# Kernel optimization log

Measured on AMD Instinct MI355X. Metric: run time of the kernel, lower is better.

Reference implementation:

```python
import jax, jax.numpy as jnp
import numpy as np

H = 12  # num_heads (ViT-B)


def setup_inputs() -> dict:
    key = jax.random.key(0)
    ks = jax.random.split(key, 16)
    B, N, C = 128, 197, 768
    eff, hd = H // 2, C // H
    d = {
        'x':  jax.random.normal(ks[0], (B, N, C), jnp.float32),
        'Wq': jax.random.normal(ks[1], (C, C), jnp.float32) * 0.02,
        'bq': jax.random.normal(ks[2], (C,), jnp.float32) * 0.02,
        'Wk': jax.random.normal(ks[3], (C, C), jnp.float32) * 0.02,
        'bk': jax.random.normal(ks[4], (C,), jnp.float32) * 0.02,
        'Wv': jax.random.normal(ks[5], (C, C), jnp.float32) * 0.02,
        'bv': jax.random.normal(ks[6], (C,), jnp.float32) * 0.02,
        'Wp': jax.random.normal(ks[7], (C, C), jnp.float32) * 0.02,
        'bp': jax.random.normal(ks[8], (C,), jnp.float32) * 0.02,
        'lq1': jax.random.normal(ks[9],  (eff, 1, hd), jnp.float32) * 0.02,
        'lk1': jax.random.normal(ks[10], (eff, 1, hd), jnp.float32) * 0.02,
        'lq2': jax.random.normal(ks[11], (eff, 1, hd), jnp.float32) * 0.02,
        'lk2': jax.random.normal(ks[12], (eff, 1, hd), jnp.float32) * 0.02,
        'num_heads': 12,
        'lambda_init': jnp.float32(0.8),
    }
    return d


def reference(x, Wq, bq, Wk, bk, Wv, bv, Wp, bp, lq1, lk1, lq2, lk2, num_heads, lambda_init):
    B, N, C = x.shape
    hd = C // num_heads
    scale = hd ** -0.5

    def heads(y):  # [B,N,C] -> [B,H,N,hd]
        return y.reshape(B, N, num_heads, hd).transpose(0, 2, 1, 3)

    q = heads(x @ Wq.T + bq)
    k = heads(x @ Wk.T + bk)
    v = heads(x @ Wv.T + bv)
    eff = num_heads // 2
    q1, q2 = q[:, :eff], q[:, eff:]
    k1, k2 = k[:, :eff], k[:, eff:]
    v1, v2 = v[:, :eff], v[:, eff:]

    l1 = jnp.exp(jnp.minimum((lq1 * lk1).sum((-1, -2)), 5.0))  # [eff]
    l2 = jnp.exp(jnp.minimum((lq2 * lk2).sum((-1, -2)), 5.0))
    lv = (l1 - l2 + lambda_init).mean()  # scalar

    def attn(qh, kh, vh):  # [B,eff,N,hd]
        s = jnp.einsum('bhnd,bhmd->bhnm', qh, kh) * scale
        a = jax.nn.softmax(s, axis=-1)
        o = jnp.einsum('bhnm,bhmd->bhnd', a, vh)
        return o.transpose(0, 2, 1, 3).reshape(B, N, C // 2)

    x1 = attn(q1, k1, v1)
    x2 = attn(q2, k2, v2)
    out = jnp.concatenate([x1 - lv * x2, x2], axis=-1)
    return out @ Wp.T + bp
```

## Files before the change

kernel.cpp:

```cpp
#include <hip/hip_runtime.h>
#include <hip/hip_bf16.h>
#include <stdint.h>


typedef __attribute__((ext_vector_type(4))) float f32x4;
typedef __attribute__((ext_vector_type(8))) short s16x8;
typedef __attribute__((ext_vector_type(8))) __bf16 bf16x8;

typedef const __attribute__((address_space(1))) void* gptr_t;
typedef __attribute__((address_space(3))) void* lptr_t;

__device__ __forceinline__ f32x4 mfma16(s16x8 a, s16x8 b, f32x4 c) {
  return __builtin_amdgcn_mfma_f32_16x16x32_bf16(
      __builtin_bit_cast(bf16x8, a), __builtin_bit_cast(bf16x8, b), c, 0, 0, 0);
}

__device__ __forceinline__ short f2bf(float f) {
  unsigned u = __float_as_uint(f);
  u += 0x7fffu + ((u >> 16) & 1u);
  return (short)(u >> 16);
}
__device__ __forceinline__ float bf2f(short s) {
  return __uint_as_float(((unsigned)(unsigned short)s) << 16);
}

__device__ __forceinline__ void gload_lds16(const void* g, void* l) {
  __builtin_amdgcn_global_load_lds((gptr_t)g, (lptr_t)l, 16, 0, 0);
}

__global__ void cvt_f32_to_bf16(const float* __restrict__ src,
                                short* __restrict__ dst, long n8) {
  long i = (long)blockIdx.x * blockDim.x + threadIdx.x;
  const long stride = (long)gridDim.x * blockDim.x;
  for (; i < n8; i += stride) {
    const float4 a = ((const float4*)src)[2 * i];
    const float4 b = ((const float4*)src)[2 * i + 1];
    s16x8 o;
    o[0] = f2bf(a.x); o[1] = f2bf(a.y); o[2] = f2bf(a.z); o[3] = f2bf(a.w);
    o[4] = f2bf(b.x); o[5] = f2bf(b.y); o[6] = f2bf(b.z); o[7] = f2bf(b.w);
    ((s16x8*)dst)[i] = o;
  }
}

__global__ void lv_kernel(const float* __restrict__ lq1, const float* __restrict__ lk1,
                          const float* __restrict__ lq2, const float* __restrict__ lk2,
                          const float* __restrict__ lambda_init, float* __restrict__ out) {
  const int l = threadIdx.x;
  float v = 0.f;
  if (l < 6) {
    float d1 = 0.f, d2 = 0.f;
    for (int j = 0; j < 64; ++j) {
      d1 += lq1[l * 64 + j] * lk1[l * 64 + j];
      d2 += lq2[l * 64 + j] * lk2[l * 64 + j];
    }
    v = expf(fminf(d1, 5.f)) - expf(fminf(d2, 5.f));
  }
  v += __shfl_xor(v, 1, 64);
  v += __shfl_xor(v, 2, 64);
  v += __shfl_xor(v, 4, 64);
  if (l == 0) out[0] = v * (1.f / 6.f) + lambda_init[0];
}

__global__ void cvt_wp_prime(const float* __restrict__ Wp,
                             const float* __restrict__ lvp,
                             short* __restrict__ dst) {
  const int idx = blockIdx.x * blockDim.x + threadIdx.x;
  if (idx >= 73728) return;
  const float lv = *lvp;
  const int ic = idx % 96;
  const float4 a = ((const float4*)Wp)[2 * idx];
  const float4 b = ((const float4*)Wp)[2 * idx + 1];
  float v[8] = {a.x, a.y, a.z, a.w, b.x, b.y, b.z, b.w};
  if (ic >= 48) {
    const float4 a2 = ((const float4*)Wp)[2 * idx - 96];
    const float4 b2 = ((const float4*)Wp)[2 * idx - 95];
    v[0] -= lv * a2.x; v[1] -= lv * a2.y; v[2] -= lv * a2.z; v[3] -= lv * a2.w;
    v[4] -= lv * b2.x; v[5] -= lv * b2.y; v[6] -= lv * b2.z; v[7] -= lv * b2.w;
  }
  s16x8 o;
#pragma unroll
  for (int j = 0; j < 8; ++j) o[j] = f2bf(v[j]);
  ((s16x8*)dst)[idx] = o;
}

template <int OUT_BF16, int NKT>
__global__ __launch_bounds__(256) void gemm_bt(const short* __restrict__ A, int lda,
                                               const short* __restrict__ B,
                                               const float* __restrict__ bias,
                                               void* __restrict__ C,
                                               int M, int N) {
  const int K = NKT * 64;
  const int nbx = N >> 7;
  const int nwg = gridDim.x;
  const int qq = nwg >> 3, rr = nwg & 7;
  const int xcd = blockIdx.x & 7, pos = blockIdx.x >> 3;
  const int wg = (xcd < rr ? xcd * (qq + 1) : rr * (qq + 1) + (xcd - rr) * qq) + pos;
  const int bx = wg % nbx;
  const int by = wg / nbx;
  const long m0 = (long)by << 7;
  const int n0 = bx << 7;
  __shared__ short Asm[128 * 64];
  __shared__ short Bsm[128 * 64];
  const int tid = threadIdx.x;
  const int lane = tid & 63;
  const int w = tid >> 6;
  const int wr = w >> 1, wc = w & 1;
  const int r16 = lane & 15, g = lane >> 4;

  const short* abase[4];
  const short* bbase[4];
#pragma unroll
  for (int i = 0; i < 4; ++i) {
    const int c = i * 256 + tid;
    const int row = c >> 3;
    const int lc = (c & 7) ^ (row & 7);
    abase[i] = A + (m0 + row) * (long)lda + lc * 8;
    bbase[i] = B + (long)(n0 + row) * (long)K + lc * 8;
  }

  f32x4 acc[4][4];
#pragma unroll
  for (int i = 0; i < 4; ++i)
#pragma unroll
    for (int j = 0; j < 4; ++j) acc[i][j] = f32x4{0.f, 0.f, 0.f, 0.f};

#pragma unroll
  for (int kt = 0; kt < NKT; ++kt) {
    __syncthreads();
#pragma unroll
    for (int i = 0; i < 4; ++i) {
      gload_lds16(abase[i] + kt * 64, Asm + i * 2048 + w * 512);
      gload_lds16(bbase[i] + kt * 64, Bsm + i * 2048 + w * 512);
    }
    asm volatile("s_waitcnt vmcnt(0)" ::: "memory");
    __syncthreads();
#pragma unroll
    for (int kk = 0; kk < 2; ++kk) {
      s16x8 av[4], bvv[4];
#pragma unroll
      for (int f = 0; f < 4; ++f) {
        const int ar = wr * 64 + f * 16 + r16;
        av[f] = *(const s16x8*)(Asm + ar * 64 + ((((kk << 2) + g) ^ (ar & 7)) << 3));
        const int br = wc * 64 + f * 16 + r16;
        bvv[f] = *(const s16x8*)(Bsm + br * 64 + ((((kk << 2) + g) ^ (br & 7)) << 3));
      }
#pragma unroll
      for (int fm = 0; fm < 4; ++fm)
#pragma unroll
        for (int fn = 0; fn < 4; ++fn)
          acc[fm][fn] = mfma16(av[fm], bvv[fn], acc[fm][fn]);
    }
  }
#pragma unroll
  for (int fm = 0; fm < 4; ++fm)
#pragma unroll
    for (int fn = 0; fn < 4; ++fn) {
      const int col = n0 + wc * 64 + fn * 16 + r16;
      const float bb = bias[col];
#pragma unroll
      for (int r = 0; r < 4; ++r) {
        const long row = m0 + wr * 64 + fm * 16 + g * 4 + r;
        const float v = acc[fm][fn][r] + bb;
        if (OUT_BF16) ((short*)C)[row * (long)N + col] = f2bf(v);
        else          ((float*)C)[row * (long)N + col] = v;
      }
    }
}

__global__ __launch_bounds__(512, 4) void attn_kernel(short* QKV) {
  const int b = blockIdx.x / 12;
  const int h = blockIdx.x % 12;
  __shared__ short Ksm[208 * 72];
  __shared__ short Vsm[64 * 232];
  __shared__ short Psm[8][2][512];
  const int tid = threadIdx.x;
  const long base = (long)b * 197 * 2304;

  for (int c = tid; c < 208 * 8; c += 512) {
    const int key = c >> 3, dch = c & 7;
    s16x8 val = {};
    if (key < 197)
      val = *(const s16x8*)(QKV + base + (long)key * 2304 + 768 + h * 64 + dch * 8);
    *(s16x8*)(Ksm + key * 72 + dch * 8) = val;
  }
  for (int c = tid; c < 224 * 8; c += 512) {
    const int key = c % 224, dch = c / 224;
    s16x8 val = {};
    if (key < 197)
      val = *(const s16x8*)(QKV + base + (long)key * 2304 + 1536 + h * 64 + dch * 8);
#pragma unroll
    for (int j = 0; j < 8; ++j) Vsm[(dch * 8 + j) * 232 + key] = val[j];
  }
  __syncthreads();

  const int lane = tid & 63, w = tid >> 6;
  const int r16 = lane & 15, g = lane >> 4;
  char* psw = (char*)Psm[w];

  for (int qt = w; qt < 13; qt += 8) {
    const int q0 = qt * 16;
    int qr = q0 + r16;
    if (qr > 196) qr = 196;
    const s16x8 qf0 = *(const s16x8*)(QKV + base + (long)qr * 2304 + h * 64 + g * 8);
    const s16x8 qf1 = *(const s16x8*)(QKV + base + (long)qr * 2304 + h * 64 + 32 + g * 8);

    f32x4 s[13];
#pragma unroll
    for (int kt = 0; kt < 13; ++kt) s[kt] = f32x4{0.f, 0.f, 0.f, 0.f};
#pragma unroll
    for (int kt = 0; kt < 13; ++kt) {
      const int krow = kt * 16 + r16;
      const s16x8 kf0 = *(const s16x8*)(Ksm + krow * 72 + g * 8);
      const s16x8 kf1 = *(const s16x8*)(Ksm + krow * 72 + 32 + g * 8);
      s[kt] = mfma16(qf0, kf0, s[kt]);
      s[kt] = mfma16(qf1, kf1, s[kt]);
    }
    float mr[4] = {-1e30f, -1e30f, -1e30f, -1e30f};
#pragma unroll
    for (int kt = 0; kt < 13; ++kt)
#pragma unroll
      for (int r = 0; r < 4; ++r) {
        float sv = s[kt][r] * 0.125f;
        if (kt == 12 && r16 >= 5) sv = -1e30f;
        s[kt][r] = sv;
        mr[r] = fmaxf(mr[r], sv);
      }
#pragma unroll
    for (int r = 0; r < 4; ++r) {
      mr[r] = fmaxf(mr[r], __shfl_xor(mr[r], 1, 64));
      mr[r] = fmaxf(mr[r], __shfl_xor(mr[r], 2, 64));
      mr[r] = fmaxf(mr[r], __shfl_xor(mr[r], 4, 64));
      mr[r] = fmaxf(mr[r], __shfl_xor(mr[r], 8, 64));
    }
    float sum[4] = {0.f, 0.f, 0.f, 0.f};
#pragma unroll
    for (int kt = 0; kt < 13; ++kt)
#pragma unroll
      for (int r = 0; r < 4; ++r) {
        const float p = __expf(s[kt][r] - mr[r]);
        s[kt][r] = p;
        sum[r] += p;
      }
#pragma unroll
    for (int r = 0; r < 4; ++r) {
      sum[r] += __shfl_xor(sum[r], 1, 64);
      sum[r] += __shfl_xor(sum[r], 2, 64);
      sum[r] += __shfl_xor(sum[r], 4, 64);
      sum[r] += __shfl_xor(sum[r], 8, 64);
    }
    f32x4 o[4];
#pragma unroll
    for (int df = 0; df < 4; ++df) o[df] = f32x4{0.f, 0.f, 0.f, 0.f};
#pragma unroll
    for (int r = 0; r < 4; ++r) {
      const int prow = g * 4 + r;
      const int sw = (prow & 7) << 4;
      *(short*)(psw + ((prow * 64 + r16 * 2) ^ sw)) = f2bf(s[0][r]);
      *(short*)(psw + ((prow * 64 + (r16 + 16) * 2) ^ sw)) = f2bf(s[1][r]);
    }
#pragma unroll
    for (int kb = 0; kb < 7; ++kb) {
      char* bufr = psw + ((kb & 1) << 10);
      char* bufw = psw + (((kb & 1) ^ 1) << 10);
      const s16x8 pa =
          *(const s16x8*)(bufr + ((r16 * 64 + g * 16) ^ ((r16 & 7) << 4)));
      if (kb < 6) {
#pragma unroll
        for (int r = 0; r < 4; ++r) {
          const int prow = g * 4 + r;
          const int sw = (prow & 7) << 4;
          const float p0f = s[2 * kb + 2][r];
          const float p1f = (kb < 5) ? s[2 * kb + 3][r] : 0.f;
          *(short*)(bufw + ((prow * 64 + r16 * 2) ^ sw)) = f2bf(p0f);
          *(short*)(bufw + ((prow * 64 + (r16 + 16) * 2) ^ sw)) = f2bf(p1f);
        }
      }
#pragma unroll
      for (int df = 0; df < 4; ++df) {
        const s16x8 vf = *(const s16x8*)(Vsm + (df * 16 + r16) * 232 + kb * 32 + g * 8);
        o[df] = mfma16(pa, vf, o[df]);
      }
    }
    float rinv[4];
#pragma unroll
    for (int r = 0; r < 4; ++r) rinv[r] = 1.f / sum[r];
#pragma unroll
    for (int df = 0; df < 4; ++df)
#pragma unroll
      for (int r = 0; r < 4; ++r) {
        const int qrow = q0 + g * 4 + r;
        if (qrow < 197)
          QKV[base + (long)qrow * 2304 + h * 64 + df * 16 + r16] =
              f2bf(o[df][r] * rinv[r]);
      }
  }
}

extern "C" void kernel_launch(void* const* d_in, const int* in_sizes, int n_in,
                              void* d_out, int out_size, void* d_ws, size_t ws_size,
                              hipStream_t stream) {
  (void)in_sizes; (void)n_in; (void)out_size; (void)ws_size;
  const float* x   = (const float*)d_in[0];
  const float* Wq  = (const float*)d_in[1];
  const float* bq  = (const float*)d_in[2];
  const float* Wk  = (const float*)d_in[3];
  const float* bk  = (const float*)d_in[4];
  const float* Wv  = (const float*)d_in[5];
  const float* bv  = (const float*)d_in[6];
  const float* Wp  = (const float*)d_in[7];
  const float* bp  = (const float*)d_in[8];
  const float* lq1 = (const float*)d_in[9];
  const float* lk1 = (const float*)d_in[10];
  const float* lq2 = (const float*)d_in[11];
  const float* lk2 = (const float*)d_in[12];
  const float* lambda_init = (const float*)d_in[14];

  char* ws = (char*)d_ws;
  short* xb   = (short*)ws;
  short* wqkv = (short*)(ws + 38731776);
  short* wpb  = (short*)(ws + 42270720);
  float* bqkv = (float*)(ws + 43450368);
  float* lvp  = (float*)(ws + 43459584);
  short* qkv  = (short*)(ws + 43459840);

  cvt_f32_to_bf16<<<2048, 256, 0, stream>>>(x, xb, 19365888 / 8);
  cvt_f32_to_bf16<<<288, 256, 0, stream>>>(Wq, wqkv, 73728);
  cvt_f32_to_bf16<<<288, 256, 0, stream>>>(Wk, wqkv + 589824, 73728);
  cvt_f32_to_bf16<<<288, 256, 0, stream>>>(Wv, wqkv + 1179648, 73728);
  lv_kernel<<<1, 64, 0, stream>>>(lq1, lk1, lq2, lk2, lambda_init, lvp);
  cvt_wp_prime<<<288, 256, 0, stream>>>(Wp, lvp, wpb);
  hipMemcpyAsync(bqkv,        bq, 768 * 4, hipMemcpyDeviceToDevice, stream);
  hipMemcpyAsync(bqkv + 768,  bk, 768 * 4, hipMemcpyDeviceToDevice, stream);
  hipMemcpyAsync(bqkv + 1536, bv, 768 * 4, hipMemcpyDeviceToDevice, stream);

  gemm_bt<1, 12><<<197 * 18, 256, 0, stream>>>(xb, 768, wqkv, bqkv, qkv,
                                               25216, 2304);
  attn_kernel<<<128 * 12, 512, 0, stream>>>(qkv);
  gemm_bt<0, 12><<<197 * 6, 256, 0, stream>>>(qkv, 2304, wpb, bp, d_out,
                                              25216, 768);
}
```

Before: 235.1 us.

## Fuse prep launches into one kernel and async-load swizzled K tile in attention

```diff
diff --git a/kernel.cpp b/kernel.cpp
--- a/kernel.cpp
+++ b/kernel.cpp
@@ -42,23 +42,51 @@
   }
 }
 
-__global__ void lv_kernel(const float* __restrict__ lq1, const float* __restrict__ lk1,
-                          const float* __restrict__ lq2, const float* __restrict__ lk2,
-                          const float* __restrict__ lambda_init, float* __restrict__ out) {
-  const int l = threadIdx.x;
-  float v = 0.f;
-  if (l < 6) {
-    float d1 = 0.f, d2 = 0.f;
-    for (int j = 0; j < 64; ++j) {
-      d1 += lq1[l * 64 + j] * lk1[l * 64 + j];
-      d2 += lq2[l * 64 + j] * lk2[l * 64 + j];
-    }
-    v = expf(fminf(d1, 5.f)) - expf(fminf(d2, 5.f));
-  }
-  v += __shfl_xor(v, 1, 64);
-  v += __shfl_xor(v, 2, 64);
-  v += __shfl_xor(v, 4, 64);
-  if (l == 0) out[0] = v * (1.f / 6.f) + lambda_init[0];
+__global__ void prep_kernel(const float* __restrict__ Wq, const float* __restrict__ Wk,
+                            const float* __restrict__ Wv, const float* __restrict__ bq,
+                            const float* __restrict__ bk, const float* __restrict__ bv,
+                            const float* __restrict__ lq1, const float* __restrict__ lk1,
+                            const float* __restrict__ lq2, const float* __restrict__ lk2,
+                            const float* __restrict__ lambda_init,
+                            short* __restrict__ wqkv, float* __restrict__ bqkv,
+                            float* __restrict__ lvp) {
+  const int blk = blockIdx.x;
+  if (blk < 864) {
+    const int which = blk / 288;
+    const int idx = (blk - which * 288) * 256 + threadIdx.x;
+    const float* src = (which == 0) ? Wq : (which == 1) ? Wk : Wv;
+    const float4 a = ((const float4*)src)[2 * idx];
+    const float4 b = ((const float4*)src)[2 * idx + 1];
+    s16x8 o;
+    o[0] = f2bf(a.x); o[1] = f2bf(a.y); o[2] = f2bf(a.z); o[3] = f2bf(a.w);
+    o[4] = f2bf(b.x); o[5] = f2bf(b.y); o[6] = f2bf(b.z); o[7] = f2bf(b.w);
+    ((s16x8*)(wqkv + which * 589824))[idx] = o;
+  } else if (blk == 864) {
+    for (int j = threadIdx.x; j < 576; j += 256) {
+      float4 v;
+      if (j < 192)      v = ((const float4*)bq)[j];
+      else if (j < 384) v = ((const float4*)bk)[j - 192];
+      else              v = ((const float4*)bv)[j - 384];
+      ((float4*)bqkv)[j] = v;
+    }
+  } else {
+    const int l = threadIdx.x;
+    if (l < 64) {
+      float v = 0.f;
+      if (l < 6) {
+        float d1 = 0.f, d2 = 0.f;
+        for (int j = 0; j < 64; ++j) {
+          d1 += lq1[l * 64 + j] * lk1[l * 64 + j];
+          d2 += lq2[l * 64 + j] * lk2[l * 64 + j];
+        }
+        v = expf(fminf(d1, 5.f)) - expf(fminf(d2, 5.f));
+      }
+      v += __shfl_xor(v, 1, 64);
+      v += __shfl_xor(v, 2, 64);
+      v += __shfl_xor(v, 4, 64);
+      if (l == 0) lvp[0] = v * (1.f / 6.f) + lambda_init[0];
+    }
+  }
 }
 
 __global__ void cvt_wp_prime(const float* __restrict__ Wp,
@@ -170,19 +198,34 @@
 __global__ __launch_bounds__(512, 4) void attn_kernel(short* QKV) {
   const int b = blockIdx.x / 12;
   const int h = blockIdx.x % 12;
-  __shared__ short Ksm[208 * 72];
+  __shared__ short Ksm[208 * 64];
   __shared__ short Vsm[64 * 232];
   __shared__ short Psm[8][2][512];
   const int tid = threadIdx.x;
   const long base = (long)b * 197 * 2304;
-
-  for (int c = tid; c < 208 * 8; c += 512) {
-    const int key = c >> 3, dch = c & 7;
-    s16x8 val = {};
-    if (key < 197)
-      val = *(const s16x8*)(QKV + base + (long)key * 2304 + 768 + h * 64 + dch * 8);
-    *(s16x8*)(Ksm + key * 72 + dch * 8) = val;
-  }
+  const int lane = tid & 63, w = tid >> 6;
+  const int r16 = lane & 15, g = lane >> 4;
+
+  int qra = w * 16 + r16;
+  const s16x8 qa0 = *(const s16x8*)(QKV + base + (long)qra * 2304 + h * 64 + g * 8);
+  const s16x8 qa1 = *(const s16x8*)(QKV + base + (long)qra * 2304 + h * 64 + 32 + g * 8);
+  s16x8 qb0 = {}, qb1 = {};
+  if (w < 5) {
+    int qrb = (w + 8) * 16 + r16;
+    if (qrb > 196) qrb = 196;
+    qb0 = *(const s16x8*)(QKV + base + (long)qrb * 2304 + h * 64 + g * 8);
+    qb1 = *(const s16x8*)(QKV + base + (long)qrb * 2304 + h * 64 + 32 + g * 8);
+  }
+
+  for (int c = tid; c < 1576; c += 512) {
+    const int row = c >> 3;
+    const int lc = (c & 7) ^ (row & 7);
+    gload_lds16(QKV + base + (long)row * 2304 + 768 + h * 64 + lc * 8,
+                Ksm + (c & ~63) * 8  + (c & 63) * 8);
+  }
+  for (int c = tid; c < 88; c += 512)
+    *(s16x8*)(Ksm + 197 * 64 + c * 8) = s16x8{};
+
   for (int c = tid; c < 224 * 8; c += 512) {
     const int key = c % 224, dch = c / 224;
     s16x8 val = {};
@@ -191,18 +234,15 @@
 #pragma unroll
     for (int j = 0; j < 8; ++j) Vsm[(dch * 8 + j) * 232 + key] = val[j];
   }
+  asm volatile("s_waitcnt vmcnt(0)" ::: "memory");
   __syncthreads();
 
-  const int lane = tid & 63, w = tid >> 6;
-  const int r16 = lane & 15, g = lane >> 4;
   char* psw = (char*)Psm[w];
 
   for (int qt = w; qt < 13; qt += 8) {
     const int q0 = qt * 16;
-    int qr = q0 + r16;
-    if (qr > 196) qr = 196;
-    const s16x8 qf0 = *(const s16x8*)(QKV + base + (long)qr * 2304 + h * 64 + g * 8);
-    const s16x8 qf1 = *(const s16x8*)(QKV + base + (long)qr * 2304 + h * 64 + 32 + g * 8);
+    const s16x8 qf0 = (qt == w) ? qa0 : qb0;
+    const s16x8 qf1 = (qt == w) ? qa1 : qb1;
 
     f32x4 s[13];
 #pragma unroll
@@ -210,8 +250,9 @@
 #pragma unroll
     for (int kt = 0; kt < 13; ++kt) {
       const int krow = kt * 16 + r16;
-      const s16x8 kf0 = *(const s16x8*)(Ksm + krow * 72 + g * 8);
-      const s16x8 kf1 = *(const s16x8*)(Ksm + krow * 72 + 32 + g * 8);
+      const int sw = krow & 7;
+      const s16x8 kf0 = *(const s16x8*)(Ksm + krow * 64 + ((g ^ sw) << 3));
+      const s16x8 kf1 = *(const s16x8*)(Ksm + krow * 64 + (((g + 4) ^ sw) << 3));
       s[kt] = mfma16(qf0, kf0, s[kt]);
       s[kt] = mfma16(qf1, kf1, s[kt]);
     }
@@ -324,14 +365,10 @@
   short* qkv  = (short*)(ws + 43459840);
 
   cvt_f32_to_bf16<<<2048, 256, 0, stream>>>(x, xb, 19365888 / 8);
-  cvt_f32_to_bf16<<<288, 256, 0, stream>>>(Wq, wqkv, 73728);
-  cvt_f32_to_bf16<<<288, 256, 0, stream>>>(Wk, wqkv + 589824, 73728);
-  cvt_f32_to_bf16<<<288, 256, 0, stream>>>(Wv, wqkv + 1179648, 73728);
-  lv_kernel<<<1, 64, 0, stream>>>(lq1, lk1, lq2, lk2, lambda_init, lvp);
+  prep_kernel<<<866, 256, 0, stream>>>(Wq, Wk, Wv, bq, bk, bv,
+                                       lq1, lk1, lq2, lk2, lambda_init,
+                                       wqkv, bqkv, lvp);
   cvt_wp_prime<<<288, 256, 0, stream>>>(Wp, lvp, wpb);
-  hipMemcpyAsync(bqkv,        bq, 768 * 4, hipMemcpyDeviceToDevice, stream);
-  hipMemcpyAsync(bqkv + 768,  bk, 768 * 4, hipMemcpyDeviceToDevice, stream);
-  hipMemcpyAsync(bqkv + 1536, bv, 768 * 4, hipMemcpyDeviceToDevice, stream);
 
   gemm_bt<1, 12><<<197 * 18, 256, 0, stream>>>(xb, 768, wqkv, bqkv, qkv,
                                                25216, 2304);
```

After: 218.4 us. 7.1% less time.
